# Optimization experiments

Hardware: AMD Instinct MI355X
Metric: run time of the kernel (lower is better)

Reference implementation:

```python
import jax, jax.numpy as jnp
import numpy as np

T = 10
EPS = 1e-05

def setup_inputs() -> dict:
    key = jax.random.key(0)
    k1, k2 = jax.random.split(key)
    B, C, H, W = 128, 64, 56, 56
    X = jax.random.normal(k1, (B, C, H, W), dtype=jnp.float32)
    beta = jnp.zeros((C,), dtype=jnp.float32)
    return {"X": X, "beta": beta}


def reference(X, beta):
    # Training-path of BWItnBlock.forward (grad enabled branch of iter_norm_batch)
    B, C, H, W = X.shape
    d = C                      # n_channels, num_groups g = 1
    m = B * H * W
    # x = X.transpose(0,1).view(g, d, -1)  -> [d, m] with g=1
    x = jnp.transpose(X, (1, 0, 2, 3)).reshape(d, m)
    mean = jnp.mean(x, axis=1, keepdims=True)          # [d, 1]
    xc = x - mean                                      # [d, m]
    I = jnp.eye(d, dtype=X.dtype)
    # Sigma = eps*I + xc xc^T / m
    Sigma = EPS * I + (xc @ xc.T) / m                  # [d, d]
    # fix_cov: multiply off-diagonal by 0.9, diagonal by 1.0
    fix = 0.9 + 0.1 * I
    Sigma = Sigma * fix
    rTr = 1.0 / jnp.trace(Sigma)                       # scalar (sum(Sigma * I))
    Sigma_N = Sigma * rTr
    # Newton-Schulz iterations for inverse sqrt: P <- 1.5 P - 0.5 P^3 Sigma_N
    P = I
    for _ in range(T):
        P = 1.5 * P - 0.5 * ((P @ P @ P) @ Sigma_N)
    wm = P * jnp.sqrt(rTr)                             # whitening matrix [d, d]
    xn = wm @ xc                                       # [d, m]
    X_hat = jnp.transpose(xn.reshape(C, B, H, W), (1, 0, 2, 3))
    X_hat = X_hat + beta.reshape(1, C, 1, 1)
    return X_hat
```

## Files before the change

kernel.cpp:

```cpp
#include <hip/hip_runtime.h>

#define CH 64
#define HW 3136
#define MTOT 401408

typedef __attribute__((ext_vector_type(8))) short short8;
typedef __attribute__((ext_vector_type(4))) float f32x4;
typedef __attribute__((ext_vector_type(4))) unsigned int u32x4;

__device__ __forceinline__ void split8(const float4 a, const float4 b,
                                       short8& hi, short8& lo, float& ssum){
  const float f[8] = {a.x,a.y,a.z,a.w, b.x,b.y,b.z,b.w};
  u32x4 hp, lp;
#pragma unroll
  for (int j=0;j<4;++j){
    const unsigned int b0 = __float_as_uint(f[2*j]);
    const unsigned int b1 = __float_as_uint(f[2*j+1]);
    hp[j] = (b0 >> 16) | (b1 & 0xFFFF0000u);
    const float h0 = __uint_as_float(b0 & 0xFFFF0000u);
    const float h1 = __uint_as_float(b1 & 0xFFFF0000u);
    const unsigned int l0 = __float_as_uint(f[2*j]   - h0);
    const unsigned int l1 = __float_as_uint(f[2*j+1] - h1);
    lp[j] = (l0 >> 16) | (l1 & 0xFFFF0000u);
  }
  hi = __builtin_bit_cast(short8, hp);
  lo = __builtin_bit_cast(short8, lp);
  ssum += ((f[0]+f[1])+(f[2]+f[3])) + ((f[4]+f[5])+(f[6]+f[7]));
}

__global__ __launch_bounds__(256) void k1_cov(const float* __restrict__ X,
                                              float* __restrict__ SR){
  constexpr int RG[10] = {0,1,1,2,2,2,3,3,3,3};
  constexpr int CG[10] = {0,0,1,0,1,2,0,1,2,3};
  __shared__ float red[4096];
  __shared__ float chs[64];

  const int t   = threadIdx.x;
  const int wid = __builtin_amdgcn_readfirstlane(t >> 6);
  const int l   = t & 63;
  const int wg  = blockIdx.x * 4 + wid;
  const int lrow = l & 15;
  const int lk   = (l >> 4) * 8;

  f32x4 acc[10];
#pragma unroll
  for (int bi=0; bi<10; ++bi) acc[bi] = (f32x4){0.f,0.f,0.f,0.f};
  float sums[4] = {0.f,0.f,0.f,0.f};

  for (int i=0; i<4; ++i){
    const int s = wg*4 + i;
    const int b = s / 98;
    const int p = (s - b*98) * 32;
    const float* base = X + (size_t)b*(CH*HW) + p + lrow*HW + lk;
    short8 fh[4], fl[4];
#pragma unroll
    for (int g=0; g<4; ++g){
      const float* pg = base + (size_t)g*16*HW;
      const float4 v0 = *(const float4*)pg;
      const float4 v1 = *(const float4*)(pg + 4);
      split8(v0, v1, fh[g], fl[g], sums[g]);
    }
#pragma unroll
    for (int bi=0; bi<10; ++bi){
      acc[bi] = __builtin_amdgcn_mfma_f32_16x16x32_bf16(fh[RG[bi]], fh[CG[bi]], acc[bi], 0,0,0);
      acc[bi] = __builtin_amdgcn_mfma_f32_16x16x32_bf16(fh[RG[bi]], fl[CG[bi]], acc[bi], 0,0,0);
      acc[bi] = __builtin_amdgcn_mfma_f32_16x16x32_bf16(fl[RG[bi]], fh[CG[bi]], acc[bi], 0,0,0);
    }
  }

#pragma unroll
  for (int g=0; g<4; ++g){
    sums[g] += __shfl_xor(sums[g], 16);
    sums[g] += __shfl_xor(sums[g], 32);
  }

  for (int w=0; w<4; ++w){
    if (wid == w){
#pragma unroll
      for (int bi=0; bi<10; ++bi){
        const int row0 = RG[bi]*16 + 4*(l>>4);
        const int col  = CG[bi]*16 + (l&15);
#pragma unroll
        for (int r=0; r<4; ++r){
          float* d = &red[(row0+r)*64 + col];
          if (w==0) *d = acc[bi][r]; else *d += acc[bi][r];
        }
      }
      if (l < 16){
#pragma unroll
        for (int g=0; g<4; ++g){
          if (w==0) chs[g*16+l] = sums[g]; else chs[g*16+l] += sums[g];
        }
      }
    }
    __syncthreads();
  }

#pragma unroll
  for (int bi=0; bi<10; ++bi){
    const int r = RG[bi]*16 + (t>>4);
    const int c = CG[bi]*16 + (t&15);
    unsafeAtomicAdd(&SR[r*64+c], red[r*64+c]);
  }
  if (t < 64) unsafeAtomicAdd(&SR[4096+t], chs[t]);
}

__device__ __forceinline__ void mm_AtB(const float* a, const float* b, float* out,
                                       float alpha, const float* aff, float beta_){
  const int t = threadIdx.x;
  const int c2 = 2*(t & 31);
  const int r0 = 8*(t >> 5);
  float acc[8][2];
#pragma unroll
  for (int i=0;i<8;++i){ acc[i][0]=0.f; acc[i][1]=0.f; }
  for (int k=0;k<64;++k){
    const float2 bv = *(const float2*)&b[k*64 + c2];
    const float4 a0 = *(const float4*)&a[k*64 + r0];
    const float4 a1 = *(const float4*)&a[k*64 + r0 + 4];
    const float av[8] = {a0.x,a0.y,a0.z,a0.w, a1.x,a1.y,a1.z,a1.w};
#pragma unroll
    for (int i=0;i<8;++i){ acc[i][0] += av[i]*bv.x; acc[i][1] += av[i]*bv.y; }
  }
  float res[8][2];
#pragma unroll
  for (int i=0;i<8;++i){
    float f0 = alpha*acc[i][0], f1 = alpha*acc[i][1];
    if (aff){ f0 += beta_*aff[(r0+i)*64 + c2]; f1 += beta_*aff[(r0+i)*64 + c2 + 1]; }
    res[i][0]=f0; res[i][1]=f1;
  }
  __syncthreads();
#pragma unroll
  for (int i=0;i<8;++i){
    float2 o2; o2.x = res[i][0]; o2.y = res[i][1];
    *(float2*)&out[(r0+i)*64 + c2] = o2;
  }
  __syncthreads();
}

__global__ __launch_bounds__(256) void k2_wm(const float* __restrict__ SR,
                                             const float* __restrict__ beta,
                                             float* __restrict__ WM,
                                             float* __restrict__ OFS){
  __shared__ __align__(16) float bufE[4096];
  __shared__ __align__(16) float bufA[4096];
  __shared__ __align__(16) float bufB[4096];
  __shared__ float meanv[64];
  __shared__ float scal[2];
  const int t = threadIdx.x;
  const float inv_m = 1.f/(float)MTOT;
  if (t < 64) meanv[t] = SR[4096 + t]*inv_m;
  __syncthreads();
  for (int idx=t; idx<4096; idx+=256){
    const int r = idx >> 6, c = idx & 63;
    const int src = ((r >> 4) >= (c >> 4)) ? idx : (c*64 + r);
    const float cov = SR[src]*inv_m - meanv[r]*meanv[c];
    bufE[idx] = (r==c) ? (cov + 1e-5f - 1.f) : 0.9f*cov;
  }
  __syncthreads();
  float n2 = 0.f, tr = 0.f;
  for (int idx=t; idx<4096; idx+=256){
    const float e = bufE[idx];
    n2 += e*e;
    if ((idx >> 6) == (idx & 63)) tr += e;
  }
  bufA[t] = n2; bufB[t] = tr;
  __syncthreads();
  if (t < 64){
    bufA[t] = bufA[t]+bufA[t+64]+bufA[t+128]+bufA[t+192];
    bufB[t] = bufB[t]+bufB[t+64]+bufB[t+128]+bufB[t+192];
  }
  __syncthreads();
  if (t == 0){
    float s1=0.f, s2=0.f;
    for (int i=0;i<64;++i){ s1 += bufA[i]; s2 += bufB[i]; }
    scal[0] = s1; scal[1] = s2;
  }
  __syncthreads();
  const float frob2 = scal[0];
  const float trE   = scal[1];
  float wscale = 1.f;
  const float* wmLds;
  if (frob2 < 0.04f){
    mm_AtB(bufE, bufE, bufA, 1.f, nullptr, 0.f);
    mm_AtB(bufA, bufE, bufB, 1.f, nullptr, 0.f);
    for (int idx=t; idx<4096; idx+=256){
      const int r = idx >> 6, c = idx & 63;
      bufB[idx] = ((r==c)?1.f:0.f) - 0.5f*bufE[idx] + 0.375f*bufA[idx] - 0.3125f*bufB[idx];
    }
    mm_AtB(bufA, bufA, bufE, 1.f, nullptr, 0.f);
    for (int idx=t; idx<4096; idx+=256)
      bufB[idx] += 0.2734375f*bufE[idx];
    wmLds = bufB;
  } else {
    const float rTr = 1.f/(trE + 64.f);
    for (int idx=t; idx<4096; idx+=256){
      const int r = idx >> 6, c = idx & 63;
      bufE[idx] = (bufE[idx] + ((r==c)?1.f:0.f))*rTr;
      bufA[idx] = (r==c)?1.f:0.f;
    }
    __syncthreads();
    for (int it=0; it<10; ++it){
      mm_AtB(bufA, bufE, bufB, 1.f, nullptr, 0.f);
      mm_AtB(bufA, bufB, bufB, 1.f, nullptr, 0.f);
      mm_AtB(bufA, bufB, bufA, -0.5f, bufA, 1.5f);
    }
    wscale = sqrtf(rTr);
    wmLds = bufA;
  }
  __syncthreads();
  for (int idx=t; idx<4096; idx+=256) WM[idx] = wmLds[idx]*wscale;
  if (t < 64){
    float d = 0.f;
    for (int j=0;j<64;++j) d += wmLds[t*64 + j]*meanv[j];
    OFS[t] = beta[t] - d*wscale;
  }
}

__global__ __launch_bounds__(256) void k3_apply(const float* __restrict__ X,
                                                const float* __restrict__ WM,
                                                const float* __restrict__ OFS,
                                                float* __restrict__ out){
  __shared__ __align__(16) float tile[64*256];
  const int t = threadIdx.x;
  const int w = __builtin_amdgcn_readfirstlane((int)(t >> 6));
  const int l = t & 63;
  const int pix = blockIdx.x*256 + 4*l;
  const int b = pix / HW;
  const int hw = pix - b*HW;
  const float* Xb = X + (size_t)b*(CH*HW) + hw;
#pragma unroll
  for (int k=0;k<16;++k){
    const int c = 4*k + w;
    const float4 v = *(const float4*)(Xb + (size_t)c*HW);
    *(float4*)&tile[c*256 + 4*l] = v;
  }
  __syncthreads();
  const int c0 = 16*w;
  float acc[16][4];
#pragma unroll
  for (int i=0;i<16;++i){ acc[i][0]=0.f; acc[i][1]=0.f; acc[i][2]=0.f; acc[i][3]=0.f; }
  for (int k=0;k<64;++k){
    const float4 xv = *(const float4*)&tile[k*256 + 4*l];
#pragma unroll
    for (int i=0;i<16;++i){
      const float wv = WM[(c0+i)*64 + k];
      acc[i][0] += wv*xv.x; acc[i][1] += wv*xv.y;
      acc[i][2] += wv*xv.z; acc[i][3] += wv*xv.w;
    }
  }
  float* ob = out + (size_t)b*(CH*HW) + hw;
#pragma unroll
  for (int i=0;i<16;++i){
    const float o = OFS[c0+i];
    float4 pk;
    pk.x = acc[i][0]+o; pk.y = acc[i][1]+o;
    pk.z = acc[i][2]+o; pk.w = acc[i][3]+o;
    *(float4*)(ob + (size_t)(c0+i)*HW) = pk;
  }
}

extern "C" void kernel_launch(void* const* d_in, const int* in_sizes, int n_in,
                              void* d_out, int out_size, void* d_ws, size_t ws_size,
                              hipStream_t stream){
  const float* X    = (const float*)d_in[0];
  const float* beta = (const float*)d_in[1];
  float* out = (float*)d_out;
  float* ws  = (float*)d_ws;
  float* SR  = ws;
  float* WM  = ws + 4160;
  float* OFS = WM + 4096;
  hipMemsetAsync(SR, 0, 4160*sizeof(float), stream);
  hipLaunchKernelGGL(k1_cov,   dim3(784),  dim3(256), 0, stream, X, SR);
  hipLaunchKernelGGL(k2_wm,    dim3(1),    dim3(256), 0, stream, SR, beta, WM, OFS);
  hipLaunchKernelGGL(k3_apply, dim3(1568), dim3(256), 0, stream, X, WM, OFS, out);
}
```

Measured before the change: 260.6 us.

## Use global_load_lds staging, transposed WM, and smaller pixel tiles in apply kernel

The apply kernel now loads X tiles directly into LDS with global_load_lds and halves the tile to 128 pixels, so the grid doubles and occupancy can rise (launch bounds 256,4). The whitening matrix is written transposed, so each k step reads a contiguous row of 16 weights, which can be fetched with wider scalar loads. Each thread now produces 2 pixels with float2 stores instead of 4 with float4, which lowers register use but gives less work per thread and narrower stores.

```diff
diff --git a/kernel.cpp b/kernel.cpp
--- a/kernel.cpp
+++ b/kernel.cpp
@@ -139,7 +139,7 @@
 
 __global__ __launch_bounds__(256) void k2_wm(const float* __restrict__ SR,
                                              const float* __restrict__ beta,
-                                             float* __restrict__ WM,
+                                             float* __restrict__ WMT,
                                              float* __restrict__ OFS){
   __shared__ __align__(16) float bufE[4096];
   __shared__ __align__(16) float bufA[4096];
@@ -208,7 +208,8 @@
     wmLds = bufA;
   }
   __syncthreads();
-  for (int idx=t; idx<4096; idx+=256) WM[idx] = wmLds[idx]*wscale;
+  for (int idx=t; idx<4096; idx+=256)
+    WMT[(idx & 63)*64 + (idx >> 6)] = wmLds[idx]*wscale;
   if (t < 64){
     float d = 0.f;
     for (int j=0;j<64;++j) d += wmLds[t*64 + j]*meanv[j];
@@ -216,46 +217,58 @@
   }
 }
 
-__global__ __launch_bounds__(256) void k3_apply(const float* __restrict__ X,
-                                                const float* __restrict__ WM,
-                                                const float* __restrict__ OFS,
-                                                float* __restrict__ out){
-  __shared__ __align__(16) float tile[64*256];
+#define PXT 128
+__global__ __launch_bounds__(256, 4) void k3_apply(const float* __restrict__ X,
+                                                   const float* __restrict__ WMT,
+                                                   const float* __restrict__ OFS,
+                                                   float* __restrict__ out){
+  __shared__ __align__(16) float tile[64*PXT];
   const int t = threadIdx.x;
   const int w = __builtin_amdgcn_readfirstlane((int)(t >> 6));
   const int l = t & 63;
-  const int pix = blockIdx.x*256 + 4*l;
-  const int b = pix / HW;
-  const int hw = pix - b*HW;
-  const float* Xb = X + (size_t)b*(CH*HW) + hw;
-#pragma unroll
-  for (int k=0;k<16;++k){
-    const int c = 4*k + w;
-    const float4 v = *(const float4*)(Xb + (size_t)c*HW);
-    *(float4*)&tile[c*256 + 4*l] = v;
-  }
-  __syncthreads();
+  const int pxbase = blockIdx.x * PXT;
+
+  {
+    const int half = l >> 5;
+    const int P    = pxbase + 4*(l & 31);
+    const int b    = P / HW;
+    const int hw   = P - b*HW;
+    const float* src0 = X + (size_t)b*(CH*HW) + hw;
+#pragma unroll
+    for (int j=0;j<8;++j){
+      const int cr = 16*w + 2*j;
+      __builtin_amdgcn_global_load_lds(
+        (const __attribute__((address_space(1))) unsigned int*)(src0 + (size_t)(cr + half)*HW),
+        (__attribute__((address_space(3))) unsigned int*)&tile[cr*PXT],
+        16, 0, 0);
+    }
+  }
+  asm volatile("s_waitcnt vmcnt(0)" ::: "memory");
+  __syncthreads();
+
   const int c0 = 16*w;
-  float acc[16][4];
-#pragma unroll
-  for (int i=0;i<16;++i){ acc[i][0]=0.f; acc[i][1]=0.f; acc[i][2]=0.f; acc[i][3]=0.f; }
+  float acc[16][2];
+#pragma unroll
+  for (int i=0;i<16;++i){ acc[i][0]=0.f; acc[i][1]=0.f; }
   for (int k=0;k<64;++k){
-    const float4 xv = *(const float4*)&tile[k*256 + 4*l];
+    const float2 xv = *(const float2*)&tile[k*PXT + 2*l];
+    const float* wr = &WMT[k*64 + c0];
 #pragma unroll
     for (int i=0;i<16;++i){
-      const float wv = WM[(c0+i)*64 + k];
-      acc[i][0] += wv*xv.x; acc[i][1] += wv*xv.y;
-      acc[i][2] += wv*xv.z; acc[i][3] += wv*xv.w;
-    }
-  }
-  float* ob = out + (size_t)b*(CH*HW) + hw;
+      acc[i][0] += wr[i]*xv.x;
+      acc[i][1] += wr[i]*xv.y;
+    }
+  }
+
+  const int P2  = pxbase + 2*l;
+  const int b2  = P2 / HW;
+  const int hw2 = P2 - b2*HW;
+  float* ob = out + (size_t)b2*(CH*HW) + hw2;
 #pragma unroll
   for (int i=0;i<16;++i){
     const float o = OFS[c0+i];
-    float4 pk;
-    pk.x = acc[i][0]+o; pk.y = acc[i][1]+o;
-    pk.z = acc[i][2]+o; pk.w = acc[i][3]+o;
-    *(float4*)(ob + (size_t)(c0+i)*HW) = pk;
+    float2 pk; pk.x = acc[i][0]+o; pk.y = acc[i][1]+o;
+    *(float2*)(ob + (size_t)(c0+i)*HW) = pk;
   }
 }
 
@@ -267,10 +280,10 @@
   float* out = (float*)d_out;
   float* ws  = (float*)d_ws;
   float* SR  = ws;
-  float* WM  = ws + 4160;
-  float* OFS = WM + 4096;
+  float* WMT = ws + 4160;
+  float* OFS = WMT + 4096;
   hipMemsetAsync(SR, 0, 4160*sizeof(float), stream);
   hipLaunchKernelGGL(k1_cov,   dim3(784),  dim3(256), 0, stream, X, SR);
-  hipLaunchKernelGGL(k2_wm,    dim3(1),    dim3(256), 0, stream, SR, beta, WM, OFS);
-  hipLaunchKernelGGL(k3_apply, dim3(1568), dim3(256), 0, stream, X, WM, OFS, out);
-}
+  hipLaunchKernelGGL(k2_wm,    dim3(1),    dim3(256), 0, stream, SR, beta, WMT, OFS);
+  hipLaunchKernelGGL(k3_apply, dim3(3136), dim3(256), 0, stream, X, WMT, OFS, out);
+}
```

Measured after the change: 250.5 us. 1.04x faster.
